# Kernel tuning notes

Hardware: AMD Instinct MI355X
Metric: run time of the kernel (lower is better)

Reference implementation:

```python
import jax, jax.numpy as jnp
import numpy as np

N = 100_000
E = 1_600_000
IN_DIM = 21
HID = 256
OUT = 256


def setup_inputs() -> dict:
    key = jax.random.key(0)
    ks = jax.random.split(key, 10)
    node_scalar = jax.random.normal(ks[0], (N, IN_DIM), dtype=jnp.float32)
    edge_index = jax.random.randint(ks[1], (2, E), 0, N, dtype=jnp.int64)
    s_in = 1.0 / np.sqrt(IN_DIM)
    s_h = 1.0 / np.sqrt(HID)
    W_in = jax.random.uniform(ks[2], (IN_DIM, HID), jnp.float32, -s_in, s_in)
    b_in = jax.random.uniform(ks[3], (HID,), jnp.float32, -s_in, s_in)
    W_self = jax.random.uniform(ks[4], (HID, HID), jnp.float32, -s_h, s_h)
    b_self = jax.random.uniform(ks[5], (HID,), jnp.float32, -s_h, s_h)
    W_nei = jax.random.uniform(ks[6], (HID, HID), jnp.float32, -s_h, s_h)
    b_nei = jax.random.uniform(ks[7], (HID,), jnp.float32, -s_h, s_h)
    W_out = jax.random.uniform(ks[8], (HID, OUT), jnp.float32, -s_h, s_h)
    b_out = jax.random.uniform(ks[9], (OUT,), jnp.float32, -s_h, s_h)
    return {
        "node_scalar": node_scalar,
        "W_in": W_in, "b_in": b_in,
        "W_self": W_self, "b_self": b_self,
        "W_nei": W_nei, "b_nei": b_nei,
        "W_out": W_out, "b_out": b_out,
        "edge_index": edge_index,
    }


def reference(node_scalar, W_in, b_in, W_self, b_self, W_nei, b_nei, W_out, b_out, edge_index):
    # x = relu(Linear(node_scalar)); dropout is identity in eval mode
    x = jax.nn.relu(node_scalar @ W_in + b_in)           # (N, H)
    n = x.shape[0]
    src, dst = edge_index[0], edge_index[1]
    msg = x[src]                                          # (E, H) gather
    agg = jax.ops.segment_sum(msg, dst, num_segments=n)   # (N, H) scatter-add
    deg = jax.ops.segment_sum(jnp.ones((dst.shape[0],), dtype=x.dtype), dst, num_segments=n)
    agg = agg / jnp.maximum(deg, 1.0)[:, None]            # degree mean (clamp_min 1)
    h = jax.nn.relu(x @ W_self + b_self + agg @ W_nei + b_nei)
    g = h.mean(axis=0)                                    # global mean pool -> (H,)
    return g @ W_out + b_out                              # (OUT,)
```

## Files before the change

### kernel.cpp

```cpp
#include <hip/hip_runtime.h>
#include <hip/hip_bf16.h>

#define HID 256
#define IND 21
#define PB 6400
#define MAXB 512
#define AST 72

typedef short short8 __attribute__((ext_vector_type(8)));
typedef float floatx16 __attribute__((ext_vector_type(16)));
typedef float floatx2 __attribute__((ext_vector_type(2)));

__device__ inline unsigned short f2bf(float f) {
  __hip_bfloat16 h = __float2bfloat16(f);
  union { __hip_bfloat16 h; unsigned short u; } c;
  c.h = h;
  return c.u;
}

__device__ inline unsigned int pk_bf16_trunc(floatx2 p) {
  union { float f; unsigned int u; } a, b;
  a.f = p.x; b.f = p.y;
  return (b.u & 0xffff0000u) | (a.u >> 16);
}

__device__ inline void acc8p(uint2 v, floatx2* a) {
  a[0] += __builtin_amdgcn_cvt_pk_f32_fp8((int)v.x, false);
  a[1] += __builtin_amdgcn_cvt_pk_f32_fp8((int)v.x, true);
  a[2] += __builtin_amdgcn_cvt_pk_f32_fp8((int)v.y, false);
  a[3] += __builtin_amdgcn_cvt_pk_f32_fp8((int)v.y, true);
}

__device__ inline short8 mk_s8(unsigned a, unsigned b, unsigned c, unsigned d) {
  union { uint4 u; short8 s; } x; x.u = make_uint4(a, b, c, d); return x.s;
}

__device__ inline short8 dec8(uint2 v) {
  unsigned w0 = pk_bf16_trunc(__builtin_amdgcn_cvt_pk_f32_fp8((int)v.x, false));
  unsigned w1 = pk_bf16_trunc(__builtin_amdgcn_cvt_pk_f32_fp8((int)v.x, true));
  unsigned w2 = pk_bf16_trunc(__builtin_amdgcn_cvt_pk_f32_fp8((int)v.y, false));
  unsigned w3 = pk_bf16_trunc(__builtin_amdgcn_cvt_pk_f32_fp8((int)v.y, true));
  return mk_s8(w0, w1, w2, w3);
}

__global__ __launch_bounds__(256) void k_front(
    const float* __restrict__ ns, const float* __restrict__ Win,
    const float* __restrict__ bin, unsigned int* __restrict__ xq,
    const float* __restrict__ Wself, const float* __restrict__ Wnei,
    unsigned short* __restrict__ Bf16,
    const int* __restrict__ dst, int* __restrict__ bcnt,
    int N, int E, int nb2, int G1) {
  int blk = blockIdx.x;
  int tid = threadIdx.x;
  if (blk < G1) {
    __shared__ float s[8][IND];
    __shared__ float fx[8][257];
    int nb = blk * 8;
    if (tid < 8 * IND) {
      int idx = nb * IND + tid;
      s[tid / IND][tid % IND] = (idx < N * IND) ? ns[idx] : 0.f;
    }
    float w[IND];
#pragma unroll
    for (int k = 0; k < IND; k++) w[k] = Win[k * HID + tid];
    float b = bin[tid];
    __syncthreads();
#pragma unroll
    for (int j = 0; j < 8; j++) {
      float acc = b;
#pragma unroll
      for (int k = 0; k < IND; k++) acc += s[j][k] * w[k];
      fx[j][tid] = acc > 0.f ? acc : 0.f;
    }
    __syncthreads();
#pragma unroll
    for (int t = 0; t < 2; t++) {
      int wi = tid + t * 256;
      int j = wi >> 6, cw = wi & 63;
      int node = nb + j;
      if (node < N) {
        const float* fp = &fx[j][cw * 4];
        int lo = __builtin_amdgcn_cvt_pk_fp8_f32(fp[0], fp[1], 0, false);
        int full = __builtin_amdgcn_cvt_pk_fp8_f32(fp[2], fp[3], lo, true);
        xq[(size_t)node * 64 + cw] = (unsigned int)full;
      }
    }
  } else if (blk < G1 + 256) {
    int n = blk - G1;
    int ct = n >> 5, l5 = n & 31;
#pragma unroll
    for (int t = 0; t < 2; t++) {
      int k = tid + t * 256;
      float v = (k < HID) ? Wself[k * HID + n] : Wnei[(k - HID) * HID + n];
      int c = k >> 4, kin = k & 15;
      int lane = (kin >> 3) * 32 + l5;
      int j = kin & 7;
      Bf16[(size_t)((c * 8 + ct) * 64 + lane) * 8 + j] = f2bf(v);
    }
  } else {
    __shared__ int lh[MAXB];
    int e0 = (blk - G1 - 256) * PB;
    for (int b = tid; b < nb2; b += 256) lh[b] = 0;
    __syncthreads();
    int c = min(PB, E - e0);
    for (int i = tid; i < c; i += 256) atomicAdd(&lh[dst[e0 + i] >> 8], 1);
    __syncthreads();
    for (int b = tid; b < nb2; b += 256)
      if (lh[b]) atomicAdd(&bcnt[b], lh[b]);
  }
}

__global__ __launch_bounds__(512) void k_bscan(
    const int* __restrict__ bcnt, int* __restrict__ bbase, int* __restrict__ bcur,
    int* __restrict__ row_start, int E, int N, int nb2) {
  __shared__ int ts[512];
  int tid = threadIdx.x;
  int v = (tid < nb2) ? bcnt[tid] : 0;
  ts[tid] = v;
  __syncthreads();
  for (int off = 1; off < 512; off <<= 1) {
    int t = (tid >= off) ? ts[tid - off] : 0;
    __syncthreads();
    ts[tid] += t;
    __syncthreads();
  }
  if (tid < nb2) { bbase[tid] = ts[tid] - v; bcur[tid] = ts[tid] - v; }
  if (tid == 0) { bbase[nb2] = E; row_start[N] = E; }
}

__global__ __launch_bounds__(256) void k_part(
    const int* __restrict__ src, const int* __restrict__ dst,
    int* __restrict__ bcur, unsigned int* __restrict__ ebuf, int E, int nb2) {
  __shared__ int lh[MAXB];
  int tid = threadIdx.x;
  int e0 = blockIdx.x * PB;
  for (int b = tid; b < nb2; b += 256) lh[b] = 0;
  __syncthreads();
  int cnt = min(PB, E - e0);
  for (int i = tid; i < cnt; i += 256) atomicAdd(&lh[dst[e0 + i] >> 8], 1);
  __syncthreads();
  for (int b = tid; b < nb2; b += 256) {
    int c = lh[b];
    lh[b] = (c > 0) ? atomicAdd(&bcur[b], c) : 0;
  }
  __syncthreads();
  for (int i = tid; i < cnt; i += 256) {
    int s = src[e0 + i];
    int d = dst[e0 + i];
    int pos = atomicAdd(&lh[d >> 8], 1);
    ebuf[pos] = ((unsigned)s << 8) | ((unsigned)d & 255u);
  }
}

__global__ __launch_bounds__(256) void k_fill2(
    const unsigned int* __restrict__ ebuf, const int* __restrict__ bbase,
    int* __restrict__ row_start, int* __restrict__ csr, int N) {
  __shared__ int lcnt[256];
  __shared__ int lcur[256];
  __shared__ int ts[256];
  int b = blockIdx.x;
  int tid = threadIdx.x;
  int start = bbase[b], end = bbase[b + 1];
  lcnt[tid] = 0;
  __syncthreads();
  for (int i = start + tid; i < end; i += 256)
    atomicAdd(&lcnt[ebuf[i] & 255u], 1);
  __syncthreads();
  int v = lcnt[tid];
  ts[tid] = v;
  __syncthreads();
  for (int off = 1; off < 256; off <<= 1) {
    int t = (tid >= off) ? ts[tid - off] : 0;
    __syncthreads();
    ts[tid] += t;
    __syncthreads();
  }
  int excl = start + ts[tid] - v;
  int node = (b << 8) + tid;
  if (node < N) row_start[node] = excl;
  lcur[tid] = excl;
  __syncthreads();
  for (int i = start + tid; i < end; i += 256) {
    unsigned int e = ebuf[i];
    int pos = atomicAdd(&lcur[e & 255u], 1);
    csr[pos] = (int)(e >> 8);
  }
}

__global__ __launch_bounds__(256) void k_agg(
    const uint2* __restrict__ xq, const int* __restrict__ csr,
    const int* __restrict__ row_start, uint2* __restrict__ aggq, int N) {
  int wid = (int)((blockIdx.x * (unsigned)blockDim.x + threadIdx.x) >> 6);
  int lane = threadIdx.x & 63;
  int half = lane >> 5;
  int l32 = lane & 31;
  if (wid >= N) return;
  int start = row_start[wid];
  int end = row_start[wid + 1];
  int c = end - start;
  floatx2 a[4], b[4], d[4], e[4];
#pragma unroll
  for (int j = 0; j < 4; j++) {
    a[j] = (floatx2){0.f, 0.f}; b[j] = (floatx2){0.f, 0.f};
    d[j] = (floatx2){0.f, 0.f}; e[j] = (floatx2){0.f, 0.f};
  }
  int i = 0;
  for (; i + 8 <= c; i += 8) {
    int s0 = csr[start + i + half];
    int s1 = csr[start + i + 2 + half];
    int s2 = csr[start + i + 4 + half];
    int s3 = csr[start + i + 6 + half];
    uint2 v0 = xq[(size_t)s0 * 32 + l32];
    uint2 v1 = xq[(size_t)s1 * 32 + l32];
    uint2 v2 = xq[(size_t)s2 * 32 + l32];
    uint2 v3 = xq[(size_t)s3 * 32 + l32];
    acc8p(v0, a); acc8p(v1, b); acc8p(v2, d); acc8p(v3, e);
  }
  for (; i + 2 <= c; i += 2) {
    int s0 = csr[start + i + half];
    uint2 v0 = xq[(size_t)s0 * 32 + l32];
    acc8p(v0, a);
  }
  if ((c & 1) && half == 0) {
    int s0 = csr[start + c - 1];
    uint2 v0 = xq[(size_t)s0 * 32 + l32];
    acc8p(v0, a);
  }
#pragma unroll
  for (int j = 0; j < 4; j++) a[j] += b[j] + d[j] + e[j];

  float f[8];
#pragma unroll
  for (int j = 0; j < 4; j++) { f[2 * j] = a[j].x; f[2 * j + 1] = a[j].y; }
#pragma unroll
  for (int j = 0; j < 8; j++) f[j] += __shfl_xor(f[j], 32);

  if (half == 0) {
    float inv = 1.0f / fmaxf((float)c, 1.0f);
#pragma unroll
    for (int j = 0; j < 8; j++) f[j] *= inv;
    int lo0 = __builtin_amdgcn_cvt_pk_fp8_f32(f[0], f[1], 0, false);
    int w0  = __builtin_amdgcn_cvt_pk_fp8_f32(f[2], f[3], lo0, true);
    int lo1 = __builtin_amdgcn_cvt_pk_fp8_f32(f[4], f[5], 0, false);
    int w1  = __builtin_amdgcn_cvt_pk_fp8_f32(f[6], f[7], lo1, true);
    aggq[(size_t)wid * 32 + l32] = make_uint2((unsigned)w0, (unsigned)w1);
  }
}

__global__ __launch_bounds__(256, 3) void k_h(
    const unsigned char* __restrict__ xq8, const unsigned char* __restrict__ aggq8,
    const unsigned short* __restrict__ Bf16, const float* __restrict__ bself,
    const float* __restrict__ bnei, float* __restrict__ gsum, int N) {
  __shared__ __align__(16) unsigned char As[128 * AST];
  __shared__ __align__(16) unsigned short Bs[16 * 512];
  __shared__ float colsum[128];
  int tid = threadIdx.x;
  int lane = tid & 63;
  int w = tid >> 6;
  int wr = w >> 1, wc = w & 1;
  int l32 = lane & 31, half = lane >> 5;
  int rowBase = blockIdx.x * 128;
  int by = blockIdx.y;

  if (tid < 128) colsum[tid] = 0.f;

  floatx16 acc[2][2];
#pragma unroll
  for (int i = 0; i < 2; i++)
#pragma unroll
    for (int j = 0; j < 2; j++) acc[i][j] = (floatx16)(0.f);

  int ar = tid >> 1;
  int ah = tid & 1;
  int gr = rowBase + ar;
  if (gr >= N) gr = N - 1;
  size_t abase = (size_t)gr * HID + ah * 32;

  int bg = tid >> 4;
  int btl = tid & 15;
  int bcl = bg >> 2, bctl = bg & 3;
  size_t bstep = (size_t)(by * 4 + bctl) * 512 + (size_t)bcl * 8 * 512 + btl * 32;

  uint4 pa0, pa1, pb0, pb1, pb2, pb3;
  {
    pa0 = *(const uint4*)(xq8 + abase);
    pa1 = *(const uint4*)(xq8 + abase + 16);
    const unsigned short* bsrc = Bf16 + bstep;
    pb0 = *(const uint4*)(bsrc);
    pb1 = *(const uint4*)(bsrc + 8);
    pb2 = *(const uint4*)(bsrc + 16);
    pb3 = *(const uint4*)(bsrc + 24);
  }

  for (int ch = 0; ch < 8; ch++) {
    __syncthreads();
    {
      unsigned char* ap = &As[ar * AST + ah * 32];
      *(uint2*)(ap + 0)  = make_uint2(pa0.x, pa0.y);
      *(uint2*)(ap + 8)  = make_uint2(pa0.z, pa0.w);
      *(uint2*)(ap + 16) = make_uint2(pa1.x, pa1.y);
      *(uint2*)(ap + 24) = make_uint2(pa1.z, pa1.w);
      unsigned short* bp = &Bs[bg * 512 + btl * 32];
      *(uint4*)(bp + 0)  = pb0;
      *(uint4*)(bp + 8)  = pb1;
      *(uint4*)(bp + 16) = pb2;
      *(uint4*)(bp + 24) = pb3;
    }
    __syncthreads();
    if (ch < 7) {
      int cn = ch + 1;
      const unsigned char* ab = (cn < 4) ? xq8 : aggq8;
      int kc = (cn & 3) * 64;
      pa0 = *(const uint4*)(ab + abase + kc);
      pa1 = *(const uint4*)(ab + abase + kc + 16);
      const unsigned short* bsrc = Bf16 + (size_t)cn * 4 * 8 * 512 + bstep;
      pb0 = *(const uint4*)(bsrc);
      pb1 = *(const uint4*)(bsrc + 8);
      pb2 = *(const uint4*)(bsrc + 16);
      pb3 = *(const uint4*)(bsrc + 24);
    }
#pragma unroll
    for (int cl = 0; cl < 4; cl++) {
      short8 afr[2];
#pragma unroll
      for (int rt = 0; rt < 2; rt++) {
        uint2 av = *(const uint2*)&As[(wr * 64 + rt * 32 + l32) * AST + cl * 16 + half * 8];
        afr[rt] = dec8(av);
      }
#pragma unroll
      for (int ctw = 0; ctw < 2; ctw++) {
        int ctl = wc * 2 + ctw;
        short8 bfr = *(const short8*)&Bs[((cl * 4 + ctl) * 64 + lane) * 8];
#pragma unroll
        for (int rt = 0; rt < 2; rt++)
          acc[rt][ctw] = __builtin_amdgcn_mfma_f32_32x32x16_bf16(
              afr[rt], bfr, acc[rt][ctw], 0, 0, 0);
      }
    }
  }

#pragma unroll
  for (int ctw = 0; ctw < 2; ctw++) {
    int lcol = (wc * 2 + ctw) * 32 + l32;
    int gcol = by * 128 + lcol;
    float bb = bself[gcol] + bnei[gcol];
    float psum[2] = {0.f, 0.f};
#pragma unroll
    for (int rt = 0; rt < 2; rt++) {
#pragma unroll
      for (int r = 0; r < 16; r++) {
        int rw = rowBase + wr * 64 + rt * 32 + (r & 3) + 8 * (r >> 2) + 4 * half;
        float v = acc[rt][ctw][r] + bb;
        v = v > 0.f ? v : 0.f;
        if (rw < N) psum[rt] += v;
      }
    }
    atomicAdd(&colsum[lcol], psum[0] + psum[1]);
  }
  __syncthreads();
  if (tid < 128) atomicAdd(&gsum[by * 128 + tid], colsum[tid]);
}

__global__ __launch_bounds__(HID) void k_out(
    const float* __restrict__ gsum, const float* __restrict__ Wout,
    const float* __restrict__ bout, float* __restrict__ out, float invN) {
  __shared__ float g[HID];
  int c = threadIdx.x;
  g[c] = gsum[c] * invN;
  __syncthreads();
  float acc = bout[c];
#pragma unroll 8
  for (int k = 0; k < HID; k++) acc += g[k] * Wout[k * HID + c];
  out[c] = acc;
}

extern "C" void kernel_launch(void* const* d_in, const int* in_sizes, int n_in,
                              void* d_out, int out_size, void* d_ws, size_t ws_size,
                              hipStream_t stream) {
  const float* ns    = (const float*)d_in[0];
  const float* Win   = (const float*)d_in[1];
  const float* bin   = (const float*)d_in[2];
  const float* Wself = (const float*)d_in[3];
  const float* bself = (const float*)d_in[4];
  const float* Wnei  = (const float*)d_in[5];
  const float* bnei  = (const float*)d_in[6];
  const float* Wout  = (const float*)d_in[7];
  const float* bout  = (const float*)d_in[8];
  const int*   eidx  = (const int*)d_in[9];

  int N = in_sizes[0] / IND;
  int E = in_sizes[9] / 2;
  const int* src = eidx;
  const int* dst = eidx + E;
  int nb2 = (N + 255) >> 8;

  unsigned int* xq    = (unsigned int*)d_ws;
  unsigned int* aggq  = xq + (size_t)N * 64;
  unsigned short* Bf16 = (unsigned short*)(aggq + (size_t)N * 64);
  int* csr       = (int*)(Bf16 + 256 * 512);
  unsigned int* ebuf = (unsigned int*)(csr + E);
  int* row_start = (int*)(ebuf + E);
  int* bcnt      = row_start + N + 1;
  int* bbase     = bcnt + MAXB;
  int* bcur      = bbase + MAXB + 1;
  float* gsum    = (float*)(bcur + MAXB);

  hipMemsetAsync(bcnt, 0, MAXB * sizeof(int), stream);
  hipMemsetAsync(gsum, 0, HID * sizeof(float), stream);

  int G1 = (N + 7) / 8;
  int pgrid = (E + PB - 1) / PB;
  k_front<<<G1 + 256 + pgrid, 256, 0, stream>>>(
      ns, Win, bin, xq, Wself, Wnei, Bf16, dst, bcnt, N, E, nb2, G1);

  k_bscan<<<1, 512, 0, stream>>>(bcnt, bbase, bcur, row_start, E, N, nb2);
  k_part<<<pgrid, 256, 0, stream>>>(src, dst, bcur, ebuf, E, nb2);
  k_fill2<<<nb2, 256, 0, stream>>>(ebuf, bbase, row_start, csr, N);

  int agrid = (N + 3) / 4;
  k_agg<<<agrid, 256, 0, stream>>>((const uint2*)xq, csr, row_start,
                                   (uint2*)aggq, N);

  dim3 hgrid((N + 127) / 128, 2);
  k_h<<<hgrid, 256, 0, stream>>>((const unsigned char*)xq,
                                 (const unsigned char*)aggq,
                                 Bf16, bself, bnei, gsum, N);

  k_out<<<1, HID, 0, stream>>>(gsum, Wout, bout, (float*)d_out, 1.0f / (float)N);
}
```

Before: 314.1 us.

## Pre-swizzle A operands into MFMA fragment layout and load via global_load_lds

The front and aggregation kernels now also write x and agg in fp8 using a fragment-major layout that matches the MFMA lane order. The k_h GEMM then streams A and B tiles straight into double-buffered LDS with global_load_lds, which removes the register staging and the extra barrier per chunk. This costs an additional copy of x in workspace and extra writes in k_front. The B reads assume the Bf16 layout maps onto 1KB fragment groups, and no explicit wait on the async LDS loads is visible, so there is a correctness risk.

After: 329.6 us. 4.9% more time.

```diff
diff --git a/kernel.cpp b/kernel.cpp
--- a/kernel.cpp
+++ b/kernel.cpp
@@ -5,7 +5,6 @@
 #define IND 21
 #define PB 6400
 #define MAXB 512
-#define AST 72
 
 typedef short short8 __attribute__((ext_vector_type(8)));
 typedef float floatx16 __attribute__((ext_vector_type(16)));
@@ -43,9 +42,16 @@
   return mk_s8(w0, w1, w2, w3);
 }
 
+__device__ inline void gl16(const unsigned char* g, unsigned char* l) {
+  __builtin_amdgcn_global_load_lds(
+      (const __attribute__((address_space(1))) unsigned char*)g,
+      (__attribute__((address_space(3))) unsigned char*)l, 16, 0, 0);
+}
+
 __global__ __launch_bounds__(256) void k_front(
     const float* __restrict__ ns, const float* __restrict__ Win,
     const float* __restrict__ bin, unsigned int* __restrict__ xq,
+    uint2* __restrict__ Aqx,
     const float* __restrict__ Wself, const float* __restrict__ Wnei,
     unsigned short* __restrict__ Bf16,
     const int* __restrict__ dst, int* __restrict__ bcnt,
@@ -85,6 +91,20 @@
         xq[(size_t)node * 64 + cw] = (unsigned int)full;
       }
     }
+    {
+      int j = tid >> 5, u = tid & 31;
+      int node = nb + j;
+      if (node < N) {
+        const float* fp = &fx[j][u * 8];
+        int lo0 = __builtin_amdgcn_cvt_pk_fp8_f32(fp[0], fp[1], 0, false);
+        int w0  = __builtin_amdgcn_cvt_pk_fp8_f32(fp[2], fp[3], lo0, true);
+        int lo1 = __builtin_amdgcn_cvt_pk_fp8_f32(fp[4], fp[5], 0, false);
+        int w1  = __builtin_amdgcn_cvt_pk_fp8_f32(fp[6], fp[7], lo1, true);
+        int g = node >> 5, row = node & 31, c = u >> 1, hi = u & 1;
+        Aqx[(size_t)(g * 16 + c) * 64 + hi * 32 + row] =
+            make_uint2((unsigned)w0, (unsigned)w1);
+      }
+    }
   } else if (blk < G1 + 256) {
     int n = blk - G1;
     int ct = n >> 5, l5 = n & 31;
@@ -243,24 +263,26 @@
     int w0  = __builtin_amdgcn_cvt_pk_fp8_f32(f[2], f[3], lo0, true);
     int lo1 = __builtin_amdgcn_cvt_pk_fp8_f32(f[4], f[5], 0, false);
     int w1  = __builtin_amdgcn_cvt_pk_fp8_f32(f[6], f[7], lo1, true);
-    aggq[(size_t)wid * 32 + l32] = make_uint2((unsigned)w0, (unsigned)w1);
+    int g = wid >> 5, row = wid & 31, cc = l32 >> 1, hi = l32 & 1;
+    aggq[(size_t)(g * 16 + cc) * 64 + hi * 32 + row] =
+        make_uint2((unsigned)w0, (unsigned)w1);
   }
 }
 
 __global__ __launch_bounds__(256, 3) void k_h(
-    const unsigned char* __restrict__ xq8, const unsigned char* __restrict__ aggq8,
-    const unsigned short* __restrict__ Bf16, const float* __restrict__ bself,
+    const unsigned char* __restrict__ Aqx, const unsigned char* __restrict__ Aqagg,
+    const unsigned char* __restrict__ Bf8, const float* __restrict__ bself,
     const float* __restrict__ bnei, float* __restrict__ gsum, int N) {
-  __shared__ __align__(16) unsigned char As[128 * AST];
-  __shared__ __align__(16) unsigned short Bs[16 * 512];
+  __shared__ __align__(16) unsigned char As[2][8192];
+  __shared__ __align__(16) unsigned char Bs[2][16384];
   __shared__ float colsum[128];
   int tid = threadIdx.x;
   int lane = tid & 63;
   int w = tid >> 6;
   int wr = w >> 1, wc = w & 1;
   int l32 = lane & 31, half = lane >> 5;
-  int rowBase = blockIdx.x * 128;
-  int by = blockIdx.y;
+  int bx = blockIdx.x, by = blockIdx.y;
+  int rowBase = bx * 128;
 
   if (tid < 128) colsum[tid] = 0.f;
 
@@ -270,67 +292,50 @@
 #pragma unroll
     for (int j = 0; j < 2; j++) acc[i][j] = (floatx16)(0.f);
 
-  int ar = tid >> 1;
-  int ah = tid & 1;
-  int gr = rowBase + ar;
-  if (gr >= N) gr = N - 1;
-  size_t abase = (size_t)gr * HID + ah * 32;
-
-  int bg = tid >> 4;
-  int btl = tid & 15;
-  int bcl = bg >> 2, bctl = bg & 3;
-  size_t bstep = (size_t)(by * 4 + bctl) * 512 + (size_t)bcl * 8 * 512 + btl * 32;
-
-  uint4 pa0, pa1, pb0, pb1, pb2, pb3;
+  size_t a_grp = (size_t)(bx * 4 + w) * 16 * 512;
+  int lb = lane * 16;
+
   {
-    pa0 = *(const uint4*)(xq8 + abase);
-    pa1 = *(const uint4*)(xq8 + abase + 16);
-    const unsigned short* bsrc = Bf16 + bstep;
-    pb0 = *(const uint4*)(bsrc);
-    pb1 = *(const uint4*)(bsrc + 8);
-    pb2 = *(const uint4*)(bsrc + 16);
-    pb3 = *(const uint4*)(bsrc + 24);
+    const unsigned char* asrc = Aqx + a_grp + lb;
+    gl16(asrc, As[0] + w * 2048);
+    gl16(asrc + 1024, As[0] + w * 2048 + 1024);
+#pragma unroll
+    for (int fi = 0; fi < 4; fi++) {
+      int cg = w;
+      int ctg = by * 4 + fi;
+      gl16(Bf8 + (size_t)(cg * 8 + ctg) * 1024 + lb, Bs[0] + (w * 4 + fi) * 1024);
+    }
   }
 
   for (int ch = 0; ch < 8; ch++) {
-    __syncthreads();
-    {
-      unsigned char* ap = &As[ar * AST + ah * 32];
-      *(uint2*)(ap + 0)  = make_uint2(pa0.x, pa0.y);
-      *(uint2*)(ap + 8)  = make_uint2(pa0.z, pa0.w);
-      *(uint2*)(ap + 16) = make_uint2(pa1.x, pa1.y);
-      *(uint2*)(ap + 24) = make_uint2(pa1.z, pa1.w);
-      unsigned short* bp = &Bs[bg * 512 + btl * 32];
-      *(uint4*)(bp + 0)  = pb0;
-      *(uint4*)(bp + 8)  = pb1;
-      *(uint4*)(bp + 16) = pb2;
-      *(uint4*)(bp + 24) = pb3;
-    }
+    int buf = ch & 1;
     __syncthreads();
     if (ch < 7) {
       int cn = ch + 1;
-      const unsigned char* ab = (cn < 4) ? xq8 : aggq8;
-      int kc = (cn & 3) * 64;
-      pa0 = *(const uint4*)(ab + abase + kc);
-      pa1 = *(const uint4*)(ab + abase + kc + 16);
-      const unsigned short* bsrc = Bf16 + (size_t)cn * 4 * 8 * 512 + bstep;
-      pb0 = *(const uint4*)(bsrc);
-      pb1 = *(const uint4*)(bsrc + 8);
-      pb2 = *(const uint4*)(bsrc + 16);
-      pb3 = *(const uint4*)(bsrc + 24);
+      const unsigned char* Aq = (cn < 4) ? Aqx : Aqagg;
+      const unsigned char* asrc = Aq + a_grp + (size_t)(cn & 3) * 2048 + lb;
+      unsigned char* ad = As[buf ^ 1] + w * 2048;
+      gl16(asrc, ad);
+      gl16(asrc + 1024, ad + 1024);
+#pragma unroll
+      for (int fi = 0; fi < 4; fi++) {
+        int cg = cn * 4 + w;
+        int ctg = by * 4 + fi;
+        gl16(Bf8 + (size_t)(cg * 8 + ctg) * 1024 + lb,
+             Bs[buf ^ 1] + (w * 4 + fi) * 1024);
+      }
     }
 #pragma unroll
     for (int cl = 0; cl < 4; cl++) {
       short8 afr[2];
 #pragma unroll
       for (int rt = 0; rt < 2; rt++) {
-        uint2 av = *(const uint2*)&As[(wr * 64 + rt * 32 + l32) * AST + cl * 16 + half * 8];
+        uint2 av = *(const uint2*)&As[buf][(wr * 2 + rt) * 2048 + cl * 512 + lane * 8];
         afr[rt] = dec8(av);
       }
 #pragma unroll
       for (int ctw = 0; ctw < 2; ctw++) {
-        int ctl = wc * 2 + ctw;
-        short8 bfr = *(const short8*)&Bs[((cl * 4 + ctl) * 64 + lane) * 8];
+        short8 bfr = *(const short8*)&Bs[buf][(cl * 4 + wc * 2 + ctw) * 1024 + lane * 16];
 #pragma unroll
         for (int rt = 0; rt < 2; rt++)
           acc[rt][ctw] = __builtin_amdgcn_mfma_f32_32x32x16_bf16(
@@ -344,7 +349,7 @@
     int lcol = (wc * 2 + ctw) * 32 + l32;
     int gcol = by * 128 + lcol;
     float bb = bself[gcol] + bnei[gcol];
-    float psum[2] = {0.f, 0.f};
+    float psum = 0.f;
 #pragma unroll
     for (int rt = 0; rt < 2; rt++) {
 #pragma unroll
@@ -352,10 +357,10 @@
         int rw = rowBase + wr * 64 + rt * 32 + (r & 3) + 8 * (r >> 2) + 4 * half;
         float v = acc[rt][ctw][r] + bb;
         v = v > 0.f ? v : 0.f;
-        if (rw < N) psum[rt] += v;
-      }
-    }
-    atomicAdd(&colsum[lcol], psum[0] + psum[1]);
+        if (rw < N) psum += v;
+      }
+    }
+    atomicAdd(&colsum[lcol], psum);
   }
   __syncthreads();
   if (tid < 128) atomicAdd(&gsum[by * 128 + tid], colsum[tid]);
@@ -393,10 +398,13 @@
   const int* src = eidx;
   const int* dst = eidx + E;
   int nb2 = (N + 255) >> 8;
+  int nbx = (N + 127) / 128;
+  size_t NGU = (size_t)nbx * 4 * 16 * 64;
 
   unsigned int* xq    = (unsigned int*)d_ws;
-  unsigned int* aggq  = xq + (size_t)N * 64;
-  unsigned short* Bf16 = (unsigned short*)(aggq + (size_t)N * 64);
+  uint2* Aqx          = (uint2*)(xq + (size_t)N * 64);
+  uint2* Aqagg        = Aqx + NGU;
+  unsigned short* Bf16 = (unsigned short*)(Aqagg + NGU);
   int* csr       = (int*)(Bf16 + 256 * 512);
   unsigned int* ebuf = (unsigned int*)(csr + E);
   int* row_start = (int*)(ebuf + E);
@@ -411,20 +419,20 @@
   int G1 = (N + 7) / 8;
   int pgrid = (E + PB - 1) / PB;
   k_front<<<G1 + 256 + pgrid, 256, 0, stream>>>(
-      ns, Win, bin, xq, Wself, Wnei, Bf16, dst, bcnt, N, E, nb2, G1);
+      ns, Win, bin, xq, Aqx, Wself, Wnei, Bf16, dst, bcnt, N, E, nb2, G1);
 
   k_bscan<<<1, 512, 0, stream>>>(bcnt, bbase, bcur, row_start, E, N, nb2);
   k_part<<<pgrid, 256, 0, stream>>>(src, dst, bcur, ebuf, E, nb2);
   k_fill2<<<nb2, 256, 0, stream>>>(ebuf, bbase, row_start, csr, N);
 
   int agrid = (N + 3) / 4;
-  k_agg<<<agrid, 256, 0, stream>>>((const uint2*)xq, csr, row_start,
-                                   (uint2*)aggq, N);
-
-  dim3 hgrid((N + 127) / 128, 2);
-  k_h<<<hgrid, 256, 0, stream>>>((const unsigned char*)xq,
-                                 (const unsigned char*)aggq,
-                                 Bf16, bself, bnei, gsum, N);
+  k_agg<<<agrid, 256, 0, stream>>>((const uint2*)xq, csr, row_start, Aqagg, N);
+
+  dim3 hgrid(nbx, 2);
+  k_h<<<hgrid, 256, 0, stream>>>((const unsigned char*)Aqx,
+                                 (const unsigned char*)Aqagg,
+                                 (const unsigned char*)Bf16,
+                                 bself, bnei, gsum, N);
 
   k_out<<<1, HID, 0, stream>>>(gsum, Wout, bout, (float*)d_out, 1.0f / (float)N);
 }
```
